# Kernel tuning notes

Hardware: AMD Instinct MI355X
Metric: run time of the kernel (lower is better)

Reference implementation:

```python
import jax, jax.numpy as jnp
import numpy as np

B, S, H = 2, 2048, 2048
E, I, TOPK = 8, 1408, 2


def setup_inputs() -> dict:
    key = jax.random.key(0)
    k0, k1, k2, k3, k4 = jax.random.split(key, 5)
    return {
        "hidden_states": jax.random.normal(k0, (B, S, H), dtype=jnp.float32),
        "Wr": jax.random.normal(k1, (H, E), dtype=jnp.float32) * 0.02,
        "Wg": jax.random.normal(k2, (E, H, I), dtype=jnp.float32) * 0.02,
        "Wu": jax.random.normal(k3, (E, H, I), dtype=jnp.float32) * 0.02,
        "Wd": jax.random.normal(k4, (E, I, H), dtype=jnp.float32) * 0.02,
    }


def reference(hidden_states, Wr, Wg, Wu, Wd):
    b, s, h = hidden_states.shape
    x = hidden_states.reshape(-1, h)                      # [T, H]
    T = x.shape[0]
    router_logits = x @ Wr                                # [T, E]
    probs = jax.nn.softmax(router_logits.astype(jnp.float32), axis=-1)
    top_w, top_i = jax.lax.top_k(probs, TOPK)             # [T, k]
    top_w = top_w / jnp.sum(top_w, axis=-1, keepdims=True)  # norm_topk_prob
    top_w = top_w.astype(x.dtype)
    # combine weights per (token, expert): zero where expert not selected
    cw = jnp.zeros((T, E), dtype=x.dtype).at[
        jnp.arange(T)[:, None], top_i].add(top_w)         # [T, E]
    # per-expert SwiGLU MLP computed densely, masked/weighted by cw
    g = jax.nn.silu(jnp.einsum('th,ehi->tei', x, Wg))     # [T, E, I]
    u = jnp.einsum('th,ehi->tei', x, Wu)                  # [T, E, I]
    y = jnp.einsum('tei,eih->teh', g * u, Wd)             # [T, E, H]
    out = jnp.einsum('te,teh->th', cw, y)                 # [T, H]
    return out.reshape(b, s, h), router_logits
```

## Files before the change

kernel.cpp:

```cpp
#include <hip/hip_runtime.h>

#define T_TOK 4096
#define HD 2048
#define NE 8
#define NI 1408

typedef __bf16 bf16x8 __attribute__((ext_vector_type(8)));
typedef float f32x4 __attribute__((ext_vector_type(4)));
typedef unsigned short ushort8 __attribute__((ext_vector_type(8)));

#define S_WAITCNT_VMCNT(n) asm volatile("s_waitcnt vmcnt(" #n ")" ::: "memory")
__device__ __forceinline__ void wave_barrier() {
  asm volatile("" ::: "memory");
  __builtin_amdgcn_s_barrier();
  asm volatile("" ::: "memory");
}

__device__ __forceinline__ unsigned short f2bf(float f) {
  unsigned int u = __float_as_uint(f);
  u += 0x7FFFu + ((u >> 16) & 1u);
  return (unsigned short)(u >> 16);
}
__device__ __forceinline__ float bf2f(unsigned short u) {
  return __uint_as_float((unsigned int)u << 16);
}

__device__ __forceinline__ void gload_lds16(const void* g, void* l) {
  __builtin_amdgcn_global_load_lds(
      (const __attribute__((address_space(1))) unsigned int*)g,
      (__attribute__((address_space(3))) unsigned int*)l, 16, 0, 0);
}

__global__ void transpose_cvt2_kernel(const float* __restrict__ srcA,
                                      unsigned short* __restrict__ dstA,
                                      const float* __restrict__ srcB,
                                      unsigned short* __restrict__ dstB,
                                      int R, int C, int dual) {
  int z = blockIdx.z;
  int e = dual ? (z >> 1) : z;
  const float* sp = (dual && (z & 1)) ? srcB : srcA;
  unsigned short* dp = (dual && (z & 1)) ? dstB : dstA;
  int c0 = blockIdx.x * 64, r0 = blockIdx.y * 128;
  const float* s = sp + (size_t)e * R * C;
  unsigned short* d = dp + (size_t)e * R * C;
  int tid = threadIdx.x;
  int tj = tid & 15, ti = tid >> 4;
  const float* sb = s + (size_t)(r0 + ti * 8) * C + c0 + tj * 4;
  f32x4 v[8];
#pragma unroll
  for (int r = 0; r < 8; r++) v[r] = *(const f32x4*)(sb + (size_t)r * C);
  unsigned short* db = d + (size_t)(c0 + tj * 4) * R + r0 + ti * 8;
#pragma unroll
  for (int cc = 0; cc < 4; cc++) {
    ushort8 o;
#pragma unroll
    for (int r = 0; r < 8; r++) o[r] = f2bf(v[r][cc]);
    *(ushort8*)(db + (size_t)cc * R) = o;
  }
}

__global__ void router_kernel(const float* __restrict__ x,
                              const float* __restrict__ Wr,
                              float* __restrict__ logits,
                              unsigned short* __restrict__ xbf,
                              int4* __restrict__ tokinfo,
                              int* __restrict__ cnt) {
  int wv = threadIdx.x >> 6, lane = threadIdx.x & 63;
  int t = blockIdx.x * 4 + wv;
  const float* xr = x + (size_t)t * HD;
  unsigned short* xbr = xbf + (size_t)t * HD;
  float acc[NE];
#pragma unroll
  for (int e = 0; e < NE; e++) acc[e] = 0.f;
  for (int hi = 0; hi < HD / 256; hi++) {
    int h = hi * 256 + lane * 4;
    f32x4 xv = *(const f32x4*)(xr + h);
    ushort4 o = { f2bf(xv[0]), f2bf(xv[1]), f2bf(xv[2]), f2bf(xv[3]) };
    *(ushort4*)(xbr + h) = o;
#pragma unroll
    for (int j = 0; j < 4; j++) {
      const float4* w4 = (const float4*)(Wr + (size_t)(h + j) * NE);
      float4 a = w4[0], b = w4[1];
      float xs = xv[j];
      acc[0] += xs * a.x; acc[1] += xs * a.y; acc[2] += xs * a.z; acc[3] += xs * a.w;
      acc[4] += xs * b.x; acc[5] += xs * b.y; acc[6] += xs * b.z; acc[7] += xs * b.w;
    }
  }
#pragma unroll
  for (int m = 32; m > 0; m >>= 1) {
#pragma unroll
    for (int e = 0; e < NE; e++) acc[e] += __shfl_xor(acc[e], m, 64);
  }
  if (lane < NE) logits[(size_t)t * NE + lane] = acc[lane];
  if (lane == 0) {
    int e0 = 0;
#pragma unroll
    for (int e = 1; e < NE; e++) if (acc[e] > acc[e0]) e0 = e;
    int e1 = (e0 == 0) ? 1 : 0;
#pragma unroll
    for (int e = 0; e < NE; e++) if (e != e0 && acc[e] > acc[e1]) e1 = e;
    float ex = expf(acc[e1] - acc[e0]);
    float w0 = 1.f / (1.f + ex);
    float w1 = ex / (1.f + ex);
    atomicAdd(&cnt[e0], 1);
    atomicAdd(&cnt[e1], 1);
    tokinfo[t] = make_int4(e0, e1, __float_as_int(w0), __float_as_int(w1));
  }
}

__global__ void route_finalize_kernel(const int4* __restrict__ tokinfo,
                                      int* __restrict__ cnt,
                                      int* __restrict__ row_tok,
                                      int2* __restrict__ tok2row) {
  if (threadIdx.x == 0) {
    int o = 0;
    for (int e = 0; e < NE; e++) { cnt[8 + e] = o; o += cnt[e]; }
  }
  __syncthreads();
  for (int t = threadIdx.x; t < T_TOK; t += 1024) {
    int4 info = tokinfo[t];
    int p0 = atomicAdd(&cnt[16 + info.x], 1);
    int r0 = cnt[8 + info.x] + p0;
    row_tok[r0] = t;
    int p1 = atomicAdd(&cnt[16 + info.y], 1);
    int r1 = cnt[8 + info.y] + p1;
    row_tok[r1] = t;
    tok2row[t] = make_int2(r0, r1);
  }
}

__launch_bounds__(256, 2)
__global__ void gemm1_kernel(const unsigned short* __restrict__ xbf,
                             const unsigned short* __restrict__ Wgt,
                             const unsigned short* __restrict__ Wut,
                             unsigned short* __restrict__ act,
                             const int* __restrict__ row_tok,
                             const int* __restrict__ cnt) {
  const int f = blockIdx.x + 11 * (blockIdx.y + 32 * blockIdx.z);
  const int e = f & 7;
  const int rem = f >> 3;
  const int nt = rem >> 5;
  const int mt = rem & 31;
  const int c = cnt[e];
  if (mt * 128 >= c) return;
  const int off = cnt[8 + e];
  const int rowbase = off + mt * 128, rowend = off + c;
  const int i0 = nt * 128;
  __shared__ __align__(16) char smem[73728];
  const int lane = threadIdx.x & 63, w = threadIdx.x >> 6;
  const int wr = w >> 1, wc = w & 1;

  const int rr0 = w * 16 + (lane >> 2);
  const int rr1 = rr0 + 64;
  const int q0 = (lane & 3) ^ ((rr0 >> 1) & 3);
  const int q1 = (lane & 3) ^ ((rr1 >> 1) & 3);
  int g0 = rowbase + rr0; if (g0 > rowend - 1) g0 = rowend - 1;
  int g1 = rowbase + rr1; if (g1 > rowend - 1) g1 = rowend - 1;
  const size_t tokA0 = (size_t)row_tok[g0] * HD;
  const size_t tokA1 = (size_t)row_tok[g1] * HD;
  const size_t bB0 = ((size_t)e * NI + i0 + rr0) * HD;
  const size_t bB1 = ((size_t)e * NI + i0 + rr1) * HD;
  const int ldsA = w * 1024;

  f32x4 zero = {0.f, 0.f, 0.f, 0.f};
  f32x4 accg[4][4], accu[4][4];
#pragma unroll
  for (int a = 0; a < 4; a++)
#pragma unroll
    for (int b = 0; b < 4; b++) { accg[a][b] = zero; accu[a][b] = zero; }

  auto stage = [&](int buf, int ks) {
    const int k0 = ks * 32;
    char* base = smem + buf * 24576;
    gload_lds16(xbf + tokA0 + k0 + q0 * 8, base + ldsA);
    gload_lds16(xbf + tokA1 + k0 + q1 * 8, base + ldsA + 4096);
    gload_lds16(Wgt + bB0 + k0 + q0 * 8, base + 8192 + ldsA);
    gload_lds16(Wgt + bB1 + k0 + q1 * 8, base + 8192 + ldsA + 4096);
    gload_lds16(Wut + bB0 + k0 + q0 * 8, base + 16384 + ldsA);
    gload_lds16(Wut + bB1 + k0 + q1 * 8, base + 16384 + ldsA + 4096);
  };
  const int rl = lane & 15, kslot = lane >> 4;
  auto compute = [&](int buf) {
    const char* base = smem + buf * 24576;
    bf16x8 af[4], bg[4], bu[4];
#pragma unroll
    for (int mi = 0; mi < 4; mi++) {
      int r = wr * 64 + mi * 16 + rl;
      int byt = r * 64 + ((kslot ^ ((r >> 1) & 3)) << 4);
      af[mi] = *(const bf16x8*)(base + byt);
    }
#pragma unroll
    for (int ni = 0; ni < 4; ni++) {
      int r = wc * 64 + ni * 16 + rl;
      int byt = r * 64 + ((kslot ^ ((r >> 1) & 3)) << 4);
      bg[ni] = *(const bf16x8*)(base + 8192 + byt);
      bu[ni] = *(const bf16x8*)(base + 16384 + byt);
    }
#pragma unroll
    for (int mi = 0; mi < 4; mi++)
#pragma unroll
      for (int ni = 0; ni < 4; ni++) {
        accg[mi][ni] = __builtin_amdgcn_mfma_f32_16x16x32_bf16(af[mi], bg[ni], accg[mi][ni], 0, 0, 0);
        accu[mi][ni] = __builtin_amdgcn_mfma_f32_16x16x32_bf16(af[mi], bu[ni], accu[mi][ni], 0, 0, 0);
      }
  };

  stage(0, 0);
  stage(1, 1);
  const int NKS = HD / 32;
  for (int ks = 0; ks < NKS; ks++) {
    if (ks + 2 < NKS) {
      stage((ks + 2) % 3, ks + 2);
      S_WAITCNT_VMCNT(12);
    } else if (ks + 1 < NKS) {
      S_WAITCNT_VMCNT(6);
    } else {
      S_WAITCNT_VMCNT(0);
    }
    wave_barrier();
    compute(ks % 3);
    wave_barrier();
  }

  const int rh = lane >> 4;
#pragma unroll
  for (int mi = 0; mi < 4; mi++)
#pragma unroll
    for (int ni = 0; ni < 4; ni++)
#pragma unroll
      for (int j = 0; j < 4; j++) {
        int grow = rowbase + wr * 64 + mi * 16 + rh * 4 + j;
        if (grow < rowend) {
          int gcol = i0 + wc * 64 + ni * 16 + rl;
          float g = accg[mi][ni][j], u = accu[mi][ni][j];
          float val = g / (1.f + __expf(-g)) * u;
          act[(size_t)grow * NI + gcol] = f2bf(val);
        }
      }
}

__launch_bounds__(256, 3)
__global__ void gemm2_kernel(const unsigned short* __restrict__ act,
                             const unsigned short* __restrict__ Wdt,
                             unsigned short* __restrict__ y,
                             const int* __restrict__ cnt) {
  const int f = blockIdx.x + 16 * (blockIdx.y + 32 * blockIdx.z);
  const int e = f & 7;
  const int rem = f >> 3;
  const int nt = rem >> 5;
  const int mt = rem & 31;
  const int c = cnt[e];
  if (mt * 128 >= c) return;
  const int off = cnt[8 + e];
  const int rowbase = off + mt * 128, rowend = off + c;
  const int n0 = nt * 128;
  __shared__ __align__(16) char smem[49152];
  const int lane = threadIdx.x & 63, w = threadIdx.x >> 6;
  const int wr = w >> 1, wc = w & 1;

  const int rr0 = w * 16 + (lane >> 2);
  const int rr1 = rr0 + 64;
  const int q0 = (lane & 3) ^ ((rr0 >> 1) & 3);
  const int q1 = (lane & 3) ^ ((rr1 >> 1) & 3);
  int g0 = rowbase + rr0; if (g0 > rowend - 1) g0 = rowend - 1;
  int g1 = rowbase + rr1; if (g1 > rowend - 1) g1 = rowend - 1;
  const size_t aA0 = (size_t)g0 * NI;
  const size_t aA1 = (size_t)g1 * NI;
  const size_t bB0 = ((size_t)e * HD + n0 + rr0) * NI;
  const size_t bB1 = ((size_t)e * HD + n0 + rr1) * NI;
  const int ldsA = w * 1024;

  f32x4 zero = {0.f, 0.f, 0.f, 0.f};
  f32x4 acc[4][4];
#pragma unroll
  for (int a = 0; a < 4; a++)
#pragma unroll
    for (int b = 0; b < 4; b++) acc[a][b] = zero;

  auto stage = [&](int buf, int ks) {
    const int k0 = ks * 32;
    char* base = smem + buf * 16384;
    gload_lds16(act + aA0 + k0 + q0 * 8, base + ldsA);
    gload_lds16(act + aA1 + k0 + q1 * 8, base + ldsA + 4096);
    gload_lds16(Wdt + bB0 + k0 + q0 * 8, base + 8192 + ldsA);
    gload_lds16(Wdt + bB1 + k0 + q1 * 8, base + 8192 + ldsA + 4096);
  };
  const int rl = lane & 15, kslot = lane >> 4;
  auto compute = [&](int buf) {
    const char* base = smem + buf * 16384;
    bf16x8 af[4], bf[4];
#pragma unroll
    for (int mi = 0; mi < 4; mi++) {
      int r = wr * 64 + mi * 16 + rl;
      int byt = r * 64 + ((kslot ^ ((r >> 1) & 3)) << 4);
      af[mi] = *(const bf16x8*)(base + byt);
    }
#pragma unroll
    for (int ni = 0; ni < 4; ni++) {
      int r = wc * 64 + ni * 16 + rl;
      int byt = r * 64 + ((kslot ^ ((r >> 1) & 3)) << 4);
      bf[ni] = *(const bf16x8*)(base + 8192 + byt);
    }
#pragma unroll
    for (int mi = 0; mi < 4; mi++)
#pragma unroll
      for (int ni = 0; ni < 4; ni++)
        acc[mi][ni] = __builtin_amdgcn_mfma_f32_16x16x32_bf16(af[mi], bf[ni], acc[mi][ni], 0, 0, 0);
  };

  stage(0, 0);
  stage(1, 1);
  const int NKS = NI / 32;
  for (int ks = 0; ks < NKS; ks++) {
    if (ks + 2 < NKS) {
      stage((ks + 2) % 3, ks + 2);
      S_WAITCNT_VMCNT(8);
    } else if (ks + 1 < NKS) {
      S_WAITCNT_VMCNT(4);
    } else {
      S_WAITCNT_VMCNT(0);
    }
    wave_barrier();
    compute(ks % 3);
    wave_barrier();
  }

  const int rh = lane >> 4;
#pragma unroll
  for (int mi = 0; mi < 4; mi++)
#pragma unroll
    for (int ni = 0; ni < 4; ni++)
#pragma unroll
      for (int j = 0; j < 4; j++) {
        int grow = rowbase + wr * 64 + mi * 16 + rh * 4 + j;
        if (grow < rowend) {
          int gcol = n0 + wc * 64 + ni * 16 + rl;
          y[(size_t)grow * HD + gcol] = f2bf(acc[mi][ni][j]);
        }
      }
}

__global__ void combine_kernel(const unsigned short* __restrict__ y,
                               const int2* __restrict__ tok2row,
                               const int4* __restrict__ tokinfo,
                               float* __restrict__ out) {
  int t = blockIdx.x, tid = threadIdx.x;
  int2 rr = tok2row[t];
  int4 info = tokinfo[t];
  float w0 = __int_as_float(info.z), w1 = __int_as_float(info.w);
  ushort8 a = ((const ushort8*)(y + (size_t)rr.x * HD))[tid];
  ushort8 b = ((const ushort8*)(y + (size_t)rr.y * HD))[tid];
  float4 o0, o1;
  o0.x = w0 * bf2f(a[0]) + w1 * bf2f(b[0]);
  o0.y = w0 * bf2f(a[1]) + w1 * bf2f(b[1]);
  o0.z = w0 * bf2f(a[2]) + w1 * bf2f(b[2]);
  o0.w = w0 * bf2f(a[3]) + w1 * bf2f(b[3]);
  o1.x = w0 * bf2f(a[4]) + w1 * bf2f(b[4]);
  o1.y = w0 * bf2f(a[5]) + w1 * bf2f(b[5]);
  o1.z = w0 * bf2f(a[6]) + w1 * bf2f(b[6]);
  o1.w = w0 * bf2f(a[7]) + w1 * bf2f(b[7]);
  float4* op = (float4*)(out + (size_t)t * HD + tid * 8);
  op[0] = o0; op[1] = o1;
}

extern "C" void kernel_launch(void* const* d_in, const int* in_sizes, int n_in,
                              void* d_out, int out_size, void* d_ws, size_t ws_size,
                              hipStream_t stream) {
  const float* x  = (const float*)d_in[0];
  const float* Wr = (const float*)d_in[1];
  const float* Wg = (const float*)d_in[2];
  const float* Wu = (const float*)d_in[3];
  const float* Wd = (const float*)d_in[4];
  float* out = (float*)d_out;
  char* ws = (char*)d_ws;

  unsigned short* xbf = (unsigned short*)(ws);
  unsigned short* Wgt = (unsigned short*)(ws + 16777216);
  unsigned short* Wut = (unsigned short*)(ws + 62914560);
  unsigned short* Wdt = (unsigned short*)(ws + 109051904);
  unsigned short* act = (unsigned short*)(ws + 155189248);
  unsigned short* yb  = (unsigned short*)(ws + 16777216);
  int4*  tokinfo      = (int4*)(ws + 178257920);
  int*   row_tok      = (int*)(ws + 178323456);
  int2*  tok2row      = (int2*)(ws + 178356224);
  int*   cnt          = (int*)(ws + 178388992);

  hipMemsetAsync(cnt, 0, 128, stream);

  router_kernel<<<T_TOK / 4, 256, 0, stream>>>(x, Wr, out + (size_t)T_TOK * HD, xbf, tokinfo, cnt);
  route_finalize_kernel<<<1, 1024, 0, stream>>>(tokinfo, cnt, row_tok, tok2row);

  transpose_cvt2_kernel<<<dim3(NI / 64, HD / 128, NE * 2), 256, 0, stream>>>(
      Wg, Wgt, Wu, Wut, HD, NI, 1);
  transpose_cvt2_kernel<<<dim3(HD / 64, NI / 128, NE), 256, 0, stream>>>(
      Wd, Wdt, nullptr, nullptr, NI, HD, 0);

  gemm1_kernel<<<dim3(11, 32, NE), 256, 0, stream>>>(xbf, Wgt, Wut, act, row_tok, cnt);
  gemm2_kernel<<<dim3(16, 32, NE), 256, 0, stream>>>(act, Wdt, yb, cnt);
  combine_kernel<<<T_TOK, 256, 0, stream>>>(yb, tok2row, tokinfo, out);
}
```

Baseline: 462.0 us.

## Merge router and weight transposes into one prepass; single barrier per k-step

Fuses the router kernel and both weight transpose/convert kernels into one launch, with block ranges selecting each role, which saves launch gaps and lets the different tasks overlap. In both GEMM kernels the k-loop now waits for the current stage, takes one barrier, and only then issues the prefetch two stages ahead, which removes the second barrier per iteration. Issuing the prefetch after the barrier keeps the triple buffer safe without the trailing barrier, but it shortens the prefetch lead time.

```diff
diff --git a/kernel.cpp b/kernel.cpp
--- a/kernel.cpp
+++ b/kernel.cpp
@@ -31,18 +31,9 @@
       (__attribute__((address_space(3))) unsigned int*)l, 16, 0, 0);
 }
 
-__global__ void transpose_cvt2_kernel(const float* __restrict__ srcA,
-                                      unsigned short* __restrict__ dstA,
-                                      const float* __restrict__ srcB,
-                                      unsigned short* __restrict__ dstB,
-                                      int R, int C, int dual) {
-  int z = blockIdx.z;
-  int e = dual ? (z >> 1) : z;
-  const float* sp = (dual && (z & 1)) ? srcB : srcA;
-  unsigned short* dp = (dual && (z & 1)) ? dstB : dstA;
-  int c0 = blockIdx.x * 64, r0 = blockIdx.y * 128;
-  const float* s = sp + (size_t)e * R * C;
-  unsigned short* d = dp + (size_t)e * R * C;
+__device__ __forceinline__ void transpose_body(const float* s,
+                                               unsigned short* d,
+                                               int R, int C, int r0, int c0) {
   int tid = threadIdx.x;
   int tj = tid & 15, ti = tid >> 4;
   const float* sb = s + (size_t)(r0 + ti * 8) * C + c0 + tj * 4;
@@ -59,52 +50,77 @@
   }
 }
 
-__global__ void router_kernel(const float* __restrict__ x,
-                              const float* __restrict__ Wr,
-                              float* __restrict__ logits,
-                              unsigned short* __restrict__ xbf,
-                              int4* __restrict__ tokinfo,
-                              int* __restrict__ cnt) {
-  int wv = threadIdx.x >> 6, lane = threadIdx.x & 63;
-  int t = blockIdx.x * 4 + wv;
-  const float* xr = x + (size_t)t * HD;
-  unsigned short* xbr = xbf + (size_t)t * HD;
-  float acc[NE];
-#pragma unroll
-  for (int e = 0; e < NE; e++) acc[e] = 0.f;
-  for (int hi = 0; hi < HD / 256; hi++) {
-    int h = hi * 256 + lane * 4;
-    f32x4 xv = *(const f32x4*)(xr + h);
-    ushort4 o = { f2bf(xv[0]), f2bf(xv[1]), f2bf(xv[2]), f2bf(xv[3]) };
-    *(ushort4*)(xbr + h) = o;
-#pragma unroll
-    for (int j = 0; j < 4; j++) {
-      const float4* w4 = (const float4*)(Wr + (size_t)(h + j) * NE);
-      float4 a = w4[0], b = w4[1];
-      float xs = xv[j];
-      acc[0] += xs * a.x; acc[1] += xs * a.y; acc[2] += xs * a.z; acc[3] += xs * a.w;
-      acc[4] += xs * b.x; acc[5] += xs * b.y; acc[6] += xs * b.z; acc[7] += xs * b.w;
-    }
-  }
-#pragma unroll
-  for (int m = 32; m > 0; m >>= 1) {
-#pragma unroll
-    for (int e = 0; e < NE; e++) acc[e] += __shfl_xor(acc[e], m, 64);
-  }
-  if (lane < NE) logits[(size_t)t * NE + lane] = acc[lane];
-  if (lane == 0) {
-    int e0 = 0;
-#pragma unroll
-    for (int e = 1; e < NE; e++) if (acc[e] > acc[e0]) e0 = e;
-    int e1 = (e0 == 0) ? 1 : 0;
-#pragma unroll
-    for (int e = 0; e < NE; e++) if (e != e0 && acc[e] > acc[e1]) e1 = e;
-    float ex = expf(acc[e1] - acc[e0]);
-    float w0 = 1.f / (1.f + ex);
-    float w1 = ex / (1.f + ex);
-    atomicAdd(&cnt[e0], 1);
-    atomicAdd(&cnt[e1], 1);
-    tokinfo[t] = make_int4(e0, e1, __float_as_int(w0), __float_as_int(w1));
+__global__ void prepass_kernel(const float* __restrict__ x,
+                               const float* __restrict__ Wr,
+                               const float* __restrict__ Wg,
+                               const float* __restrict__ Wu,
+                               const float* __restrict__ Wd,
+                               float* __restrict__ logits,
+                               unsigned short* __restrict__ xbf,
+                               unsigned short* __restrict__ Wgt,
+                               unsigned short* __restrict__ Wut,
+                               unsigned short* __restrict__ Wdt,
+                               int4* __restrict__ tokinfo,
+                               int* __restrict__ cnt) {
+  const int bid = blockIdx.x;
+  if (bid < 1024) {
+    int wv = threadIdx.x >> 6, lane = threadIdx.x & 63;
+    int t = bid * 4 + wv;
+    const float* xr = x + (size_t)t * HD;
+    unsigned short* xbr = xbf + (size_t)t * HD;
+    float acc[NE];
+#pragma unroll
+    for (int e = 0; e < NE; e++) acc[e] = 0.f;
+    for (int hi = 0; hi < HD / 256; hi++) {
+      int h = hi * 256 + lane * 4;
+      f32x4 xv = *(const f32x4*)(xr + h);
+      ushort4 o = { f2bf(xv[0]), f2bf(xv[1]), f2bf(xv[2]), f2bf(xv[3]) };
+      *(ushort4*)(xbr + h) = o;
+#pragma unroll
+      for (int j = 0; j < 4; j++) {
+        const float4* w4 = (const float4*)(Wr + (size_t)(h + j) * NE);
+        float4 a = w4[0], b = w4[1];
+        float xs = xv[j];
+        acc[0] += xs * a.x; acc[1] += xs * a.y; acc[2] += xs * a.z; acc[3] += xs * a.w;
+        acc[4] += xs * b.x; acc[5] += xs * b.y; acc[6] += xs * b.z; acc[7] += xs * b.w;
+      }
+    }
+#pragma unroll
+    for (int m = 32; m > 0; m >>= 1) {
+#pragma unroll
+      for (int e = 0; e < NE; e++) acc[e] += __shfl_xor(acc[e], m, 64);
+    }
+    if (lane < NE) logits[(size_t)t * NE + lane] = acc[lane];
+    if (lane == 0) {
+      int e0 = 0;
+#pragma unroll
+      for (int e = 1; e < NE; e++) if (acc[e] > acc[e0]) e0 = e;
+      int e1 = (e0 == 0) ? 1 : 0;
+#pragma unroll
+      for (int e = 0; e < NE; e++) if (e != e0 && acc[e] > acc[e1]) e1 = e;
+      float ex = expf(acc[e1] - acc[e0]);
+      float w0 = 1.f / (1.f + ex);
+      float w1 = ex / (1.f + ex);
+      atomicAdd(&cnt[e0], 1);
+      atomicAdd(&cnt[e1], 1);
+      tokinfo[t] = make_int4(e0, e1, __float_as_int(w0), __float_as_int(w1));
+    }
+  } else if (bid < 1024 + 5632) {
+    int r = bid - 1024;
+    int xt = r % 22; r /= 22;
+    int yt = r % 16; r /= 16;
+    int e = r >> 1, sel = r & 1;
+    const float* sp = (sel ? Wu : Wg) + (size_t)e * HD * NI;
+    unsigned short* dp = (sel ? Wut : Wgt) + (size_t)e * HD * NI;
+    transpose_body(sp, dp, HD, NI, yt * 128, xt * 64);
+  } else {
+    int r = bid - 1024 - 5632;
+    int xt = r % 32; r /= 32;
+    int yt = r % 11; r /= 11;
+    int e = r;
+    const float* sp = Wd + (size_t)e * NI * HD;
+    unsigned short* dp = Wdt + (size_t)e * NI * HD;
+    transpose_body(sp, dp, NI, HD, yt * 128, xt * 64);
   }
 }
 
@@ -209,17 +225,14 @@
   stage(1, 1);
   const int NKS = HD / 32;
   for (int ks = 0; ks < NKS; ks++) {
-    if (ks + 2 < NKS) {
-      stage((ks + 2) % 3, ks + 2);
-      S_WAITCNT_VMCNT(12);
-    } else if (ks + 1 < NKS) {
+    if (ks < NKS - 1) {
       S_WAITCNT_VMCNT(6);
     } else {
       S_WAITCNT_VMCNT(0);
     }
     wave_barrier();
+    if (ks + 2 < NKS) stage((ks + 2) % 3, ks + 2);
     compute(ks % 3);
-    wave_barrier();
   }
 
   const int rh = lane >> 4;
@@ -312,17 +325,14 @@
   stage(1, 1);
   const int NKS = NI / 32;
   for (int ks = 0; ks < NKS; ks++) {
-    if (ks + 2 < NKS) {
-      stage((ks + 2) % 3, ks + 2);
-      S_WAITCNT_VMCNT(8);
-    } else if (ks + 1 < NKS) {
+    if (ks < NKS - 1) {
       S_WAITCNT_VMCNT(4);
     } else {
       S_WAITCNT_VMCNT(0);
     }
     wave_barrier();
+    if (ks + 2 < NKS) stage((ks + 2) % 3, ks + 2);
     compute(ks % 3);
-    wave_barrier();
   }
 
   const int rh = lane >> 4;
@@ -387,13 +397,10 @@
 
   hipMemsetAsync(cnt, 0, 128, stream);
 
-  router_kernel<<<T_TOK / 4, 256, 0, stream>>>(x, Wr, out + (size_t)T_TOK * HD, xbf, tokinfo, cnt);
+  prepass_kernel<<<1024 + 5632 + 2816, 256, 0, stream>>>(
+      x, Wr, Wg, Wu, Wd, out + (size_t)T_TOK * HD, xbf, Wgt, Wut, Wdt,
+      tokinfo, cnt);
   route_finalize_kernel<<<1, 1024, 0, stream>>>(tokinfo, cnt, row_tok, tok2row);
-
-  transpose_cvt2_kernel<<<dim3(NI / 64, HD / 128, NE * 2), 256, 0, stream>>>(
-      Wg, Wgt, Wu, Wut, HD, NI, 1);
-  transpose_cvt2_kernel<<<dim3(HD / 64, NI / 128, NE), 256, 0, stream>>>(
-      Wd, Wdt, nullptr, nullptr, NI, HD, 0);
 
   gemm1_kernel<<<dim3(11, 32, NE), 256, 0, stream>>>(xbf, Wgt, Wut, act, row_tok, cnt);
   gemm2_kernel<<<dim3(16, 32, NE), 256, 0, stream>>>(act, Wdt, yb, cnt);
```

New measurement: 441.5 us. 1.05x faster.
